# Kernel optimization log

Hardware: AMD Instinct MI355X
Metric: run time of the kernel (lower is better)

## Reference

```python
import jax, jax.numpy as jnp
import numpy as np

NEG_SLOPE = 0.01
EPS = 1e-8


def _conv2d(x, w, b, pad):
    y = jax.lax.conv_general_dilated(
        x, w, window_strides=(1, 1), padding=[(pad, pad), (pad, pad)],
        dimension_numbers=("NCHW", "OIHW", "NCHW"))
    return y + b[None, :, None, None]


def _leaky(x):
    return jnp.where(x >= 0, x, NEG_SLOPE * x)


def _maxpool2(x):
    return jax.lax.reduce_window(x, -jnp.inf, jax.lax.max,
                                 (1, 1, 2, 2), (1, 1, 2, 2), "VALID")


def _upsample2(x):  # nearest, scale_factor=2 (matches F.interpolate default)
    return jnp.repeat(jnp.repeat(x, 2, axis=2), 2, axis=3)


def _forward(x1, x2, pts1, enc, dec):
    B, L = pts1.shape[:2]
    H, W = x1.shape[-2:]
    h1, h2 = x1, x2
    pts = pts1.astype(jnp.int32)
    attns, feats = [], []
    for (w, b) in enc:
        Hi, Wi = h1.shape[-2:]
        h1 = _leaky(_conv2d(h1, w, b, 2))
        h2 = _leaky(_conv2d(h2, w, b, 2))
        feats.append(h2)
        h1 = _maxpool2(h1)
        h2 = _maxpool2(h2)
        C_, Hi_, Wi_ = h1.shape[-3:]
        # pts[...,0] = pts[...,0]*Hi_//Hi ; same for W (integer floor)
        pts = jnp.stack([(pts[..., 0] * Hi_) // Hi, (pts[..., 1] * Wi_) // Wi], axis=-1)
        idx = pts[..., 0] * Wi_ + pts[..., 1]  # (B, L)
        h1f = h1.reshape(B, C_, Hi_ * Wi_)
        h2f = h2.reshape(B, C_, Hi_ * Wi_)
        query = jnp.take_along_axis(h1f, jnp.broadcast_to(idx[:, None, :], (B, C_, L)), axis=2)  # (B, C, L)
        # cosine similarity between every pixel of h2 and every query point
        dots = jnp.einsum("bcp,bcl->bpl", h2f, query)
        n2 = jnp.maximum(jnp.linalg.norm(h2f, axis=1), EPS)    # (B, P)
        nq = jnp.maximum(jnp.linalg.norm(query, axis=1), EPS)  # (B, L)
        attn = dots / (n2[:, :, None] * nq[:, None, :])        # (B, P, L)
        attn = attn.reshape(B, Hi_, Wi_, L).transpose(0, 3, 1, 2).reshape(B * L, 1, Hi_, Wi_)
        attns.append(attn)
    h2 = jnp.tile(h2, (L, 1, 1, 1))  # torch .repeat(L,1,1,1)
    n_dec = len(dec)
    for i, (w, b) in enumerate(dec):
        j = len(enc) - i - 1
        h2 = jnp.concatenate([h2, attns[j]], axis=1)
        h2 = _upsample2(h2)
        feat = jnp.tile(feats[j], (L, 1, 1, 1))
        h2 = jnp.concatenate([h2, feat], axis=1)
        h2 = _conv2d(h2, w, b, 1)
        if i < n_dec - 1:
            h2 = _leaky(h2)
    return h2.reshape(B, L, H, W)


def setup_inputs() -> dict:
    key = jax.random.key(0)
    ks = jax.random.split(key, 24)
    B, L, H, W = 2, 32, 256, 256
    inp = {
        "x1": jax.random.uniform(ks[0], (B, 3, H, W), dtype=jnp.float32),
        "x2": jax.random.uniform(ks[1], (B, 3, H, W), dtype=jnp.float32),
        "pts1": jax.random.randint(ks[2], (B, L, 2), 0, H, dtype=jnp.int32),
    }
    enc_shapes = [(4, 3), (8, 4), (16, 8), (16, 16)]
    dec_shapes = [(16, 33), (8, 33), (4, 17), (1, 9)]
    k = 3
    for i, (co, ci) in enumerate(enc_shapes):
        inp[f"enc_w{i}"] = jax.random.normal(ks[k], (co, ci, 5, 5), dtype=jnp.float32) * 0.05
        inp[f"enc_b{i}"] = jnp.zeros((co,), dtype=jnp.float32)
        k += 1
    for i, (co, ci) in enumerate(dec_shapes):
        inp[f"dec_w{i}"] = jax.random.normal(ks[k], (co, ci, 3, 3), dtype=jnp.float32) * 0.05
        inp[f"dec_b{i}"] = jnp.zeros((co,), dtype=jnp.float32)
        k += 1
    return inp


def reference(x1, x2, pts1,
              enc_w0, enc_b0, enc_w1, enc_b1, enc_w2, enc_b2, enc_w3, enc_b3,
              dec_w0, dec_b0, dec_w1, dec_b1, dec_w2, dec_b2, dec_w3, dec_b3):
    enc = [(enc_w0, enc_b0), (enc_w1, enc_b1), (enc_w2, enc_b2), (enc_w3, enc_b3)]
    dec = [(dec_w0, dec_b0), (dec_w1, dec_b1), (dec_w2, dec_b2), (dec_w3, dec_b3)]
    return _forward(x1, x2, pts1, enc, dec)
```

## Files before the change

### kernel.cpp

```cpp
#include <hip/hip_runtime.h>
#include <cstdint>

__device__ __forceinline__ float leaky(float v) { return v >= 0.f ? v : 0.01f * v; }

__global__ void __launch_bounds__(256) enc0_k(
    const float* __restrict__ x1, const float* __restrict__ x2,
    const float* __restrict__ w, const float* __restrict__ bias,
    float* __restrict__ c2, float* __restrict__ pout)
{
    constexpr int R = 256;
    __shared__ float ss[3 * 36 * 36];
    __shared__ float ws[4 * 3 * 25 + 4];
    int t = threadIdx.x;
    int n = blockIdx.y;
    int tileY = blockIdx.x >> 3, tileX = blockIdx.x & 7;
    int Y0 = 32 * tileY, X0 = 32 * tileX;
    const float* src = (n < 2) ? x1 + (size_t)n * 3 * R * R
                               : x2 + (size_t)(n - 2) * 3 * R * R;

    for (int i = t; i < 300; i += 256) ws[i] = w[i];
    if (t < 4) ws[300 + t] = bias[t];
    for (int ci = 0; ci < 3; ++ci) {
        const float* sp = src + (size_t)ci * R * R;
        for (int i = t; i < 1296; i += 256) {
            int r = i / 36, col = i - r * 36;
            int gy = Y0 - 2 + r, gx = X0 - 2 + col;
            float v = 0.f;
            if (gy >= 0 && gy < R && gx >= 0 && gx < R) v = sp[gy * R + gx];
            ss[ci * 1296 + i] = v;
        }
    }
    __syncthreads();

    int qx = t & 15, qy = t >> 4;
    float acc[4][2][2];
#pragma unroll
    for (int co = 0; co < 4; ++co) {
        float b0 = ws[300 + co];
        acc[co][0][0] = b0; acc[co][0][1] = b0; acc[co][1][0] = b0; acc[co][1][1] = b0;
    }
#pragma unroll
    for (int ci = 0; ci < 3; ++ci) {
        const float* sp = &ss[ci * 1296 + (2 * qy) * 36 + 2 * qx];
        float S[6][6];
#pragma unroll
        for (int i = 0; i < 6; ++i)
#pragma unroll
            for (int j = 0; j < 6; ++j) S[i][j] = sp[i * 36 + j];
#pragma unroll
        for (int co = 0; co < 4; ++co) {
#pragma unroll
            for (int dy = 0; dy < 5; ++dy) {
#pragma unroll
                for (int dx = 0; dx < 5; ++dx) {
                    float wv = ws[(co * 3 + ci) * 25 + dy * 5 + dx];
                    acc[co][0][0] = fmaf(wv, S[dy][dx],         acc[co][0][0]);
                    acc[co][0][1] = fmaf(wv, S[dy][dx + 1],     acc[co][0][1]);
                    acc[co][1][0] = fmaf(wv, S[dy + 1][dx],     acc[co][1][0]);
                    acc[co][1][1] = fmaf(wv, S[dy + 1][dx + 1], acc[co][1][1]);
                }
            }
        }
    }
#pragma unroll
    for (int co = 0; co < 4; ++co) {
        float v00 = leaky(acc[co][0][0]), v01 = leaky(acc[co][0][1]);
        float v10 = leaky(acc[co][1][0]), v11 = leaky(acc[co][1][1]);
        if (n >= 2) {
            float* op = c2 + ((size_t)((n - 2) * 4 + co)) * R * R + (Y0 + 2 * qy) * R + X0 + 2 * qx;
            float2 a; a.x = v00; a.y = v01; *(float2*)op = a;
            float2 b2; b2.x = v10; b2.y = v11; *(float2*)(op + R) = b2;
        }
        float pv = fmaxf(fmaxf(v00, v01), fmaxf(v10, v11));
        pout[((size_t)(n * 4 + co)) * 16384 + (16 * tileY + qy) * 128 + 16 * tileX + qx] = pv;
    }
}

template<int R, int CI, int CO, int COG>
__global__ void __launch_bounds__(256) enc_k(
    const float* __restrict__ src1, const float* __restrict__ src2,
    const float* __restrict__ w, const float* __restrict__ bias,
    float* __restrict__ c2, float* __restrict__ pout)
{
    constexpr int W = R, H = R, Wt = R / 2;
    constexpr int RPB = 256 / Wt;
    __shared__ float ws[COG * CI * 25];
    __shared__ float pl[(RPB / 2) * COG * Wt];

    int t = threadIdx.x;
    int gid = blockIdx.x * 256 + t;
    int col = gid % Wt;
    int y = (gid / Wt) % H;
    int n = (gid / (Wt * H)) & 3;
    int g = gid / (Wt * H * 4);

    for (int i = t; i < COG * CI * 25; i += 256) ws[i] = w[g * COG * CI * 25 + i];
    __syncthreads();

    const float* sp = (n < 2) ? (src1 + (size_t)n * CI * H * W)
                              : (src2 + (size_t)(n - 2) * CI * H * W);
    int x0 = col * 2;

    float acc[COG][2];
#pragma unroll
    for (int cg = 0; cg < COG; ++cg) { float b0 = bias[g * COG + cg]; acc[cg][0] = b0; acc[cg][1] = b0; }

    bool okr[5], okc[3];
#pragma unroll
    for (int i = 0; i < 5; ++i) { int yy = y + i - 2; okr[i] = (yy >= 0) && (yy < H); }
#pragma unroll
    for (int j = 0; j < 3; ++j) { int xx = x0 + 2 * j - 2; okc[j] = (xx >= 0) && (xx < W); }

#pragma unroll 4
    for (int ci = 0; ci < CI; ++ci) {
        const float* s = sp + ci * H * W + (y - 2) * W + (x0 - 2);
        float p[5][6];
#pragma unroll
        for (int i = 0; i < 5; ++i) {
#pragma unroll
            for (int j = 0; j < 3; ++j) {
                if (okr[i] & okc[j]) {
                    float2 v = *(const float2*)(s + i * W + 2 * j);
                    p[i][2 * j] = v.x; p[i][2 * j + 1] = v.y;
                } else { p[i][2 * j] = 0.f; p[i][2 * j + 1] = 0.f; }
            }
        }
#pragma unroll
        for (int cg = 0; cg < COG; ++cg) {
#pragma unroll
            for (int dy = 0; dy < 5; ++dy) {
#pragma unroll
                for (int dx = 0; dx < 5; ++dx) {
                    float wv = ws[(cg * CI + ci) * 25 + dy * 5 + dx];
                    acc[cg][0] = fmaf(wv, p[dy][dx],     acc[cg][0]);
                    acc[cg][1] = fmaf(wv, p[dy][dx + 1], acc[cg][1]);
                }
            }
        }
    }

    int r = t / Wt;
    float m[COG];
#pragma unroll
    for (int cg = 0; cg < COG; ++cg) {
        float v0 = leaky(acc[cg][0]), v1 = leaky(acc[cg][1]);
        m[cg] = fmaxf(v0, v1);
        if (n >= 2) {
            float2 stv; stv.x = v0; stv.y = v1;
            *(float2*)(c2 + ((size_t)((n - 2) * CO + g * COG + cg)) * H * W + y * W + x0) = stv;
        }
    }
    if (r & 1) {
#pragma unroll
        for (int cg = 0; cg < COG; ++cg)
            pl[((r >> 1) * COG + cg) * Wt + col] = m[cg];
    }
    __syncthreads();
    if (!(r & 1)) {
#pragma unroll
        for (int cg = 0; cg < COG; ++cg) {
            float pv = fmaxf(m[cg], pl[((r >> 1) * COG + cg) * Wt + col]);
            pout[((size_t)(n * CO + g * COG + cg)) * Wt * Wt + (y >> 1) * Wt + col] = pv;
        }
    }
}

template<int C, int RP, int SHIFT>
__device__ __forceinline__ void attn_body(
    const float* __restrict__ pool, const int* __restrict__ pts,
    float* __restrict__ out, int tile, int b)
{
    constexpr int P = RP * RP;
    __shared__ float qs[32 * C];
    int t = threadIdx.x;
    if (t < 32) {
        int l = t;
        int py = pts[(b * 32 + l) * 2 + 0] >> SHIFT;
        int px = pts[(b * 32 + l) * 2 + 1] >> SHIFT;
        const float* qp = pool + (size_t)(b * C) * P + py * RP + px;
        float v[C]; float s = 0.f;
#pragma unroll
        for (int c = 0; c < C; ++c) { v[c] = qp[c * P]; s += v[c] * v[c]; }
        float invn = 1.f / fmaxf(sqrtf(s), 1e-8f);
#pragma unroll
        for (int c = 0; c < C; ++c) qs[l * C + c] = v[c] * invn;
    }
    __syncthreads();
    int p = tile * 256 + t;
    const float* hp = pool + (size_t)((2 + b) * C) * P + p;
    float v[C]; float s = 0.f;
#pragma unroll
    for (int c = 0; c < C; ++c) { v[c] = hp[c * P]; s += v[c] * v[c]; }
    float invn2 = 1.f / fmaxf(sqrtf(s), 1e-8f);
#pragma unroll 4
    for (int l = 0; l < 32; ++l) {
        float d = 0.f;
#pragma unroll
        for (int c = 0; c < C; ++c) d = fmaf(v[c], qs[l * C + c], d);
        out[(size_t)(b * 32 + l) * P + p] = d * invn2;
    }
}

__global__ void __launch_bounds__(256) attn_all_k(
    const float* __restrict__ p0, const float* __restrict__ p1,
    const float* __restrict__ p2, const float* __restrict__ p3,
    const int* __restrict__ pts,
    float* __restrict__ at0, float* __restrict__ at1,
    float* __restrict__ at2, float* __restrict__ at3)
{
    int bx = blockIdx.x;
    if (bx < 128)      attn_body<4, 128, 1>(p0, pts, at0, bx >> 1, bx & 1);
    else if (bx < 160) { int r = bx - 128; attn_body<8, 64, 2>(p1, pts, at1, r >> 1, r & 1); }
    else if (bx < 168) { int r = bx - 160; attn_body<16, 32, 3>(p2, pts, at2, r >> 1, r & 1); }
    else               { int r = bx - 168; attn_body<16, 16, 4>(p3, pts, at3, r >> 1, r & 1); }
}

template<int R, int CI, int CINW, int CO, int COG>
__device__ __forceinline__ void fb_body(
    const float* __restrict__ in, const float* __restrict__ w,
    const float* __restrict__ bias, float* __restrict__ fb,
    int par, int tile, int cog)
{
    constexpr int QD = R / 2;
    __shared__ float ws[COG * CI * 9];
    int t = threadIdx.x;
    for (int i = t; i < COG * CI * 9; i += 256) {
        int co = i / (CI * 9), rem = i - co * (CI * 9);
        ws[i] = w[(cog * COG + co) * CINW * 9 + (CINW - CI) * 9 + rem];
    }
    __syncthreads();
    int q = tile * 256 + t;
    int qx = q % QD, qy = q / QD;
    const float* ip = in + (size_t)par * CI * R * R;
    float acc[COG][2][2];
#pragma unroll
    for (int co = 0; co < COG; ++co) {
        float b0 = bias[cog * COG + co];
        acc[co][0][0] = b0; acc[co][0][1] = b0; acc[co][1][0] = b0; acc[co][1][1] = b0;
    }
    bool fr[4], fc[4];
#pragma unroll
    for (int i = 0; i < 4; ++i) {
        int yy = 2 * qy - 1 + i; fr[i] = (yy >= 0) && (yy < R);
        int xx = 2 * qx - 1 + i; fc[i] = (xx >= 0) && (xx < R);
    }
#pragma unroll 4
    for (int ci = 0; ci < CI; ++ci) {
        const float* bp = ip + (size_t)ci * R * R + (2 * qy - 1) * R + (2 * qx - 1);
        float F[4][4];
#pragma unroll
        for (int i = 0; i < 4; ++i)
#pragma unroll
            for (int j = 0; j < 4; ++j)
                F[i][j] = (fr[i] & fc[j]) ? bp[i * R + j] : 0.f;
#pragma unroll
        for (int co = 0; co < COG; ++co) {
#pragma unroll
            for (int dy = 0; dy < 3; ++dy) {
#pragma unroll
                for (int dx = 0; dx < 3; ++dx) {
                    float wv = ws[(co * CI + ci) * 9 + dy * 3 + dx];
                    acc[co][0][0] = fmaf(wv, F[dy][dx],         acc[co][0][0]);
                    acc[co][0][1] = fmaf(wv, F[dy][dx + 1],     acc[co][0][1]);
                    acc[co][1][0] = fmaf(wv, F[dy + 1][dx],     acc[co][1][0]);
                    acc[co][1][1] = fmaf(wv, F[dy + 1][dx + 1], acc[co][1][1]);
                }
            }
        }
    }
#pragma unroll
    for (int co = 0; co < COG; ++co) {
        float* op = fb + ((size_t)(par * CO + cog * COG + co)) * R * R + (2 * qy) * R + 2 * qx;
        float2 a; a.x = acc[co][0][0]; a.y = acc[co][0][1]; *(float2*)op = a;
        float2 b2; b2.x = acc[co][1][0]; b2.y = acc[co][1][1]; *(float2*)(op + R) = b2;
    }
}

__device__ __forceinline__ void fb0_body(
    const float* __restrict__ p3, const float* __restrict__ c2_3,
    const float* __restrict__ w, const float* __restrict__ bias,
    float* __restrict__ fb0, int par, int tile, int cog)
{
    __shared__ float ws0[4 * 33 * 9];
    int t = threadIdx.x;
    for (int i = t; i < 4 * 33 * 9; i += 256) ws0[i] = w[cog * 4 * 33 * 9 + i];
    __syncthreads();
    int px = tile * 256 + t;
    int x = px & 31, y = px >> 5;
    const float* prevp = p3 + (size_t)(2 + par) * 16 * 256;
    const float* featp = c2_3 + (size_t)par * 16 * 1024;
    float acc[4];
#pragma unroll
    for (int co = 0; co < 4; ++co) acc[co] = bias[cog * 4 + co];

    bool oky[3], okx[3];
    int py[3], pxh[3];
#pragma unroll
    for (int i = 0; i < 3; ++i) {
        int iy = y - 1 + i; oky[i] = (iy >= 0) && (iy < 32); py[i] = (iy >= 0 ? iy : 0) >> 1;
        int ix = x - 1 + i; okx[i] = (ix >= 0) && (ix < 32); pxh[i] = (ix >= 0 ? ix : 0) >> 1;
    }
#pragma unroll 4
    for (int ci = 0; ci < 16; ++ci) {
        const float* pp = prevp + ci * 256;
        float V[3][3];
#pragma unroll
        for (int i = 0; i < 3; ++i)
#pragma unroll
            for (int j = 0; j < 3; ++j)
                V[i][j] = (oky[i] & okx[j]) ? pp[py[i] * 16 + pxh[j]] : 0.f;
#pragma unroll
        for (int co = 0; co < 4; ++co) {
#pragma unroll
            for (int tap = 0; tap < 9; ++tap)
                acc[co] = fmaf(ws0[(co * 33 + ci) * 9 + tap], V[tap / 3][tap % 3], acc[co]);
        }
    }
#pragma unroll 4
    for (int cf = 0; cf < 16; ++cf) {
        const float* fp = featp + cf * 1024;
        float F[3][3];
#pragma unroll
        for (int i = 0; i < 3; ++i)
#pragma unroll
            for (int j = 0; j < 3; ++j) {
                int iy = y - 1 + i, ix = x - 1 + j;
                F[i][j] = (oky[i] & okx[j]) ? fp[iy * 32 + ix] : 0.f;
            }
#pragma unroll
        for (int co = 0; co < 4; ++co) {
#pragma unroll
            for (int tap = 0; tap < 9; ++tap)
                acc[co] = fmaf(ws0[(co * 33 + 17 + cf) * 9 + tap], F[tap / 3][tap % 3], acc[co]);
        }
    }
#pragma unroll
    for (int co = 0; co < 4; ++co)
        fb0[((size_t)(par * 16 + cog * 4 + co)) * 1024 + y * 32 + x] = acc[co];
}

__global__ void __launch_bounds__(256) fb_all_k(
    const float* __restrict__ p3, const float* __restrict__ c2_3,
    const float* __restrict__ c2_2, const float* __restrict__ c2_1,
    const float* __restrict__ c2_0,
    const float* __restrict__ w0, const float* __restrict__ b0,
    const float* __restrict__ w1, const float* __restrict__ b1,
    const float* __restrict__ w2, const float* __restrict__ b2,
    const float* __restrict__ w3, const float* __restrict__ b3,
    float* __restrict__ fb0, float* __restrict__ fb1,
    float* __restrict__ fb2, float* __restrict__ fb3)
{
    int bx = blockIdx.x;
    if (bx < 128) {
        int sub = bx; int par = sub >> 6, tile = sub & 63;
        fb_body<256, 4, 9, 1, 1>(c2_0, w3, b3, fb3, par, tile, 0);
    } else if (bx < 160) {
        int sub = bx - 128; int par = sub >> 4, tile = sub & 15;
        fb_body<128, 8, 17, 4, 4>(c2_1, w2, b2, fb2, par, tile, 0);
    } else if (bx < 176) {
        int sub = bx - 160; int cog = sub & 1, tile = (sub >> 1) & 3, par = sub >> 3;
        fb_body<64, 16, 33, 8, 4>(c2_2, w1, b1, fb1, par, tile, cog);
    } else {
        int sub = bx - 176; int cog = sub & 3, tile = (sub >> 2) & 3, par = sub >> 4;
        fb0_body(p3, c2_3, w0, b0, fb0, par, tile, cog);
    }
}

__global__ void __launch_bounds__(256) dec0k_k(
    const float* __restrict__ at3, const float* __restrict__ fb0,
    const float* __restrict__ w, float* __restrict__ out)
{
    __shared__ float ws4[9 * 16];
    int t = threadIdx.x;
    if (t < 144) {
        int tap = t / 16, co = t - (t / 16) * 16;
        ws4[tap * 16 + co] = w[co * 33 * 9 + 16 * 9 + tap];
    }
    __syncthreads();
    int gid = blockIdx.x;
    int k = gid >> 2, tile = gid & 3;
    int px = tile * 256 + t;
    int x = px & 31, y = px >> 5;
    int par = k & 1;
    const float* ap = at3 + (size_t)k * 256;

    float A[3][3];
#pragma unroll
    for (int i = 0; i < 3; ++i) {
        int iy = y - 1 + i; bool oy = (iy >= 0) && (iy < 32); int py = (iy >= 0 ? iy : 0) >> 1;
#pragma unroll
        for (int j = 0; j < 3; ++j) {
            int ix = x - 1 + j; bool ox = (ix >= 0) && (ix < 32); int qx = (ix >= 0 ? ix : 0) >> 1;
            A[i][j] = (oy && ox) ? ap[py * 16 + qx] : 0.f;
        }
    }
    float acc[16];
#pragma unroll
    for (int co = 0; co < 16; ++co)
        acc[co] = fb0[((size_t)(par * 16 + co)) * 1024 + y * 32 + x];
#pragma unroll
    for (int tap = 0; tap < 9; ++tap) {
        float av = A[tap / 3][tap % 3];
#pragma unroll
        for (int c4 = 0; c4 < 4; ++c4) {
            float4 wv = *(const float4*)&ws4[tap * 16 + c4 * 4];
            acc[c4 * 4 + 0] = fmaf(wv.x, av, acc[c4 * 4 + 0]);
            acc[c4 * 4 + 1] = fmaf(wv.y, av, acc[c4 * 4 + 1]);
            acc[c4 * 4 + 2] = fmaf(wv.z, av, acc[c4 * 4 + 2]);
            acc[c4 * 4 + 3] = fmaf(wv.w, av, acc[c4 * 4 + 3]);
        }
    }
#pragma unroll
    for (int co = 0; co < 16; ++co)
        out[((size_t)(k * 16 + co)) * 1024 + y * 32 + x] = leaky(acc[co]);
}

__global__ void __launch_bounds__(256, 4) dec1k_k(
    const float* __restrict__ prev, const float* __restrict__ attn,
    const float* __restrict__ fb1, const float* __restrict__ w,
    float* __restrict__ out)
{
    constexpr int R = 64, CP = 16, CIN = 33, Rh = 32, CO = 8, COG = 4;
    __shared__ float ws[17 * 9 * COG];
    __shared__ float sh4[17 * 60 * 4];

    int t = threadIdx.x;
    int bz = blockIdx.y;
    int kg = bz >> 1, cog = bz & 1;
    int p = kg & 1;
    int kbase = (kg >> 1) * 8 + p;
    int tileY = blockIdx.x >> 2, tileX = blockIdx.x & 3;
    int Y0 = 8 * tileY, X0 = 16 * tileX;
    int hy0 = 4 * tileY - 1, hx0 = 8 * tileX - 1;

    for (int i = t; i < 17 * 9 * COG; i += 256) {
        int col = i & 3, idx = i >> 2;
        ws[idx * 4 + col] = w[(cog * COG + col) * CIN * 9 + idx];
    }
#pragma unroll 2
    for (int i = t; i < 17 * 60; i += 256) {
        int c = i / 60, rem = i - c * 60;
        int r = rem / 10, col = rem - r * 10;
        int gy = hy0 + r, gx = hx0 + col;
        bool ok = (gy >= 0) && (gy < Rh) && (gx >= 0) && (gx < Rh);
        int off = gy * Rh + gx;
        float4 v4; v4.x = 0.f; v4.y = 0.f; v4.z = 0.f; v4.w = 0.f;
        if (ok) {
            if (c < CP) {
                v4.x = prev[((size_t)((kbase + 0) * CP + c)) * Rh * Rh + off];
                v4.y = prev[((size_t)((kbase + 2) * CP + c)) * Rh * Rh + off];
                v4.z = prev[((size_t)((kbase + 4) * CP + c)) * Rh * Rh + off];
                v4.w = prev[((size_t)((kbase + 6) * CP + c)) * Rh * Rh + off];
            } else {
                v4.x = attn[(size_t)(kbase + 0) * Rh * Rh + off];
                v4.y = attn[(size_t)(kbase + 2) * Rh * Rh + off];
                v4.z = attn[(size_t)(kbase + 4) * Rh * Rh + off];
                v4.w = attn[(size_t)(kbase + 6) * Rh * Rh + off];
            }
        }
        *(float4*)&sh4[i * 4] = v4;
    }
    __syncthreads();

    int px = t & 127, copair = t >> 7;
    int qx = px & 15, qy = px >> 4;

    float acc[4][2];
#pragma unroll
    for (int c2 = 0; c2 < 2; ++c2) {
        float fv = fb1[((size_t)(p * CO + cog * COG + copair * 2 + c2)) * 4096 + (Y0 + qy) * R + X0 + qx];
#pragma unroll
        for (int j = 0; j < 4; ++j) acc[j][c2] = fv;
    }

    int rr[3] = {(qy + 1) >> 1, (qy + 2) >> 1, (qy + 3) >> 1};
    int cc[3] = {(qx + 1) >> 1, (qx + 2) >> 1, (qx + 3) >> 1};
    int pofs[3][3];
#pragma unroll
    for (int i = 0; i < 3; ++i)
#pragma unroll
        for (int j2 = 0; j2 < 3; ++j2)
            pofs[i][j2] = (rr[i] * 10 + cc[j2]) * 4;

#pragma unroll 4
    for (int ci = 0; ci < 17; ++ci) {
        const float* hp = &sh4[ci * 240];
        float4 P4[3][3];
#pragma unroll
        for (int i = 0; i < 3; ++i)
#pragma unroll
            for (int j2 = 0; j2 < 3; ++j2)
                P4[i][j2] = *(const float4*)&hp[pofs[i][j2]];
#pragma unroll
        for (int dy = 0; dy < 3; ++dy) {
#pragma unroll
            for (int dx = 0; dx < 3; ++dx) {
                float2 wv = *(const float2*)&ws[(ci * 9 + dy * 3 + dx) * 4 + copair * 2];
                acc[0][0] = fmaf(wv.x, P4[dy][dx].x, acc[0][0]);
                acc[1][0] = fmaf(wv.x, P4[dy][dx].y, acc[1][0]);
                acc[2][0] = fmaf(wv.x, P4[dy][dx].z, acc[2][0]);
                acc[3][0] = fmaf(wv.x, P4[dy][dx].w, acc[3][0]);
                acc[0][1] = fmaf(wv.y, P4[dy][dx].x, acc[0][1]);
                acc[1][1] = fmaf(wv.y, P4[dy][dx].y, acc[1][1]);
                acc[2][1] = fmaf(wv.y, P4[dy][dx].z, acc[2][1]);
                acc[3][1] = fmaf(wv.y, P4[dy][dx].w, acc[3][1]);
            }
        }
    }

#pragma unroll
    for (int j = 0; j < 4; ++j) {
        int k = kbase + 2 * j;
#pragma unroll
        for (int c2 = 0; c2 < 2; ++c2) {
            int co = cog * COG + copair * 2 + c2;
            out[((size_t)(k * CO + co)) * 4096 + (Y0 + qy) * R + X0 + qx] = leaky(acc[j][c2]);
        }
    }
}

template<int R, int CP, int CO, int CINW, int MINW, bool DOLEAKY>
__global__ void __launch_bounds__(256, MINW) dechalf_k(
    const float* __restrict__ prev, const float* __restrict__ attn,
    const float* __restrict__ fb, const float* __restrict__ w,
    float* __restrict__ out)
{
    constexpr int Rh = R / 2, TX = R / 16;
    constexpr bool PACKW = (CO == 4);
    __shared__ float sh[4][(CP + 1) * 100];
    __shared__ float ws4[PACKW ? (CP + 1) * 9 * 4 : 4];

    int t = threadIdx.x;
    int kg = blockIdx.y;
    int p = kg & 1;
    int kbase = (kg >> 1) * 8 + p;
    int tileY = blockIdx.x / TX, tileX = blockIdx.x % TX;
    int Y0 = 16 * tileY, X0 = 16 * tileX;
    int hy0 = 8 * tileY - 1, hx0 = 8 * tileX - 1;

    if (PACKW) {
        for (int i = t; i < (CP + 1) * 9 * 4; i += 256) {
            int co = i & 3, idx = i >> 2;
            ws4[i] = w[co * CINW * 9 + idx];
        }
    }
#pragma unroll 2
    for (int i = t; i < CP * 100; i += 256) {
        int c = i / 100, rem = i - c * 100;
        int r = rem / 10, col = rem - r * 10;
        int gy = hy0 + r, gx = hx0 + col;
        bool ok = (gy >= 0) && (gy < Rh) && (gx >= 0) && (gx < Rh);
        int off = gy * Rh + gx;
#pragma unroll
        for (int j = 0; j < 4; ++j) {
            float v = 0.f;
            if (ok) v = prev[((size_t)((kbase + 2 * j) * CP + c)) * Rh * Rh + off];
            sh[j][i] = v;
        }
    }
    if (t < 100) {
        int r = t / 10, col = t - r * 10;
        int gy = hy0 + r, gx = hx0 + col;
        bool ok = (gy >= 0) && (gy < Rh) && (gx >= 0) && (gx < Rh);
        int off = gy * Rh + gx;
#pragma unroll
        for (int j = 0; j < 4; ++j) {
            float v = 0.f;
            if (ok) v = attn[(size_t)(kbase + 2 * j) * Rh * Rh + off];
            sh[j][CP * 100 + t] = v;
        }
    }
    __syncthreads();

    int ksub = t >> 6, q = t & 63, qx = q & 7, qy = q >> 3;
    int k = kbase + 2 * ksub;

    float acc[CO][2][2];
#pragma unroll
    for (int co = 0; co < CO; ++co) {
        const float* fp = fb + ((size_t)(p * CO + co)) * R * R + (Y0 + 2 * qy) * R + X0 + 2 * qx;
        float2 r0 = *(const float2*)fp;
        float2 r1 = *(const float2*)(fp + R);
        acc[co][0][0] = r0.x; acc[co][0][1] = r0.y;
        acc[co][1][0] = r1.x; acc[co][1][1] = r1.y;
    }

#pragma unroll
    for (int ci = 0; ci < CP + 1; ++ci) {
        const float* hp = &sh[ksub][ci * 100 + qy * 10 + qx];
        float P[3][3];
#pragma unroll
        for (int i = 0; i < 3; ++i)
#pragma unroll
            for (int j = 0; j < 3; ++j) P[i][j] = hp[i * 10 + j];
#pragma unroll
        for (int dy = 0; dy < 3; ++dy) {
#pragma unroll
            for (int dx = 0; dx < 3; ++dx) {
                float p00 = P[(dy + 1) >> 1][(dx + 1) >> 1];
                float p01 = P[(dy + 1) >> 1][(dx + 2) >> 1];
                float p10 = P[(dy + 2) >> 1][(dx + 1) >> 1];
                float p11 = P[(dy + 2) >> 1][(dx + 2) >> 1];
                if (PACKW) {
                    float4 wv = *(const float4*)&ws4[(ci * 9 + dy * 3 + dx) * 4];
                    const float* wvp = (const float*)&wv;
#pragma unroll
                    for (int co = 0; co < CO; ++co) {
                        acc[co][0][0] = fmaf(wvp[co], p00, acc[co][0][0]);
                        acc[co][0][1] = fmaf(wvp[co], p01, acc[co][0][1]);
                        acc[co][1][0] = fmaf(wvp[co], p10, acc[co][1][0]);
                        acc[co][1][1] = fmaf(wvp[co], p11, acc[co][1][1]);
                    }
                } else {
                    float wv = w[ci * 9 + dy * 3 + dx];
                    acc[0][0][0] = fmaf(wv, p00, acc[0][0][0]);
                    acc[0][0][1] = fmaf(wv, p01, acc[0][0][1]);
                    acc[0][1][0] = fmaf(wv, p10, acc[0][1][0]);
                    acc[0][1][1] = fmaf(wv, p11, acc[0][1][1]);
                }
            }
        }
    }

#pragma unroll
    for (int co = 0; co < CO; ++co) {
        float v00 = acc[co][0][0], v01 = acc[co][0][1];
        float v10 = acc[co][1][0], v11 = acc[co][1][1];
        if (DOLEAKY) { v00 = leaky(v00); v01 = leaky(v01); v10 = leaky(v10); v11 = leaky(v11); }
        float* op = out + ((size_t)(k * CO + co)) * R * R + (Y0 + 2 * qy) * R + X0 + 2 * qx;
        float2 a; a.x = v00; a.y = v01; *(float2*)op = a;
        float2 b2; b2.x = v10; b2.y = v11; *(float2*)(op + R) = b2;
    }
}

extern "C" void kernel_launch(void* const* d_in, const int* in_sizes, int n_in,
                              void* d_out, int out_size, void* d_ws, size_t ws_size,
                              hipStream_t stream)
{
    (void)in_sizes; (void)n_in; (void)out_size; (void)ws_size;
    const float* x1 = (const float*)d_in[0];
    const float* x2 = (const float*)d_in[1];
    const int* pts = (const int*)d_in[2];
    const float* ew[4] = {(const float*)d_in[3], (const float*)d_in[5],
                          (const float*)d_in[7], (const float*)d_in[9]};
    const float* eb[4] = {(const float*)d_in[4], (const float*)d_in[6],
                          (const float*)d_in[8], (const float*)d_in[10]};
    const float* dw[4] = {(const float*)d_in[11], (const float*)d_in[13],
                          (const float*)d_in[15], (const float*)d_in[17]};
    const float* db[4] = {(const float*)d_in[12], (const float*)d_in[14],
                          (const float*)d_in[16], (const float*)d_in[18]};

    float* wsp = (float*)d_ws;
    size_t off = 0;
    auto A = [&](size_t n) { float* p = wsp + off; off += n; return p; };

    float* p0 = A((size_t)4 * 4 * 128 * 128);
    float* p1 = A((size_t)4 * 8 * 64 * 64);
    float* p2 = A((size_t)4 * 16 * 32 * 32);
    float* p3 = A((size_t)4 * 16 * 16 * 16);
    float* c2_0 = A((size_t)2 * 4 * 256 * 256);
    float* c2_1 = A((size_t)2 * 8 * 128 * 128);
    float* c2_2 = A((size_t)2 * 16 * 64 * 64);
    float* c2_3 = A((size_t)2 * 16 * 32 * 32);
    float* at0 = A((size_t)64 * 128 * 128);
    float* at1 = A((size_t)64 * 64 * 64);
    float* at2 = A((size_t)64 * 32 * 32);
    float* at3 = A((size_t)64 * 16 * 16);
    float* dec0 = A((size_t)64 * 16 * 32 * 32);
    float* dec1 = A((size_t)64 * 8 * 64 * 64);
    float* dec2 = A((size_t)64 * 4 * 128 * 128);
    float* fb0 = A((size_t)2 * 16 * 32 * 32);
    float* fb1 = A((size_t)2 * 8 * 64 * 64);
    float* fb2 = A((size_t)2 * 4 * 128 * 128);
    float* fb3 = A((size_t)2 * 256 * 256);
    float* outp = (float*)d_out;

    { dim3 g(64, 4); enc0_k<<<g, 256, 0, stream>>>(x1, x2, ew[0], eb[0], c2_0, p0); }
    enc_k<128, 4, 8, 2><<<512, 256, 0, stream>>>(p0, p0 + (size_t)2 * 4 * 128 * 128,
                                                 ew[1], eb[1], c2_1, p1);
    enc_k<64, 8, 16, 2><<<256, 256, 0, stream>>>(p1, p1 + (size_t)2 * 8 * 64 * 64,
                                                 ew[2], eb[2], c2_2, p2);
    enc_k<32, 16, 16, 1><<<128, 256, 0, stream>>>(p2, p2 + (size_t)2 * 16 * 32 * 32,
                                                  ew[3], eb[3], c2_3, p3);

    attn_all_k<<<170, 256, 0, stream>>>(p0, p1, p2, p3, pts, at0, at1, at2, at3);

    fb_all_k<<<208, 256, 0, stream>>>(p3, c2_3, c2_2, c2_1, c2_0,
                                      dw[0], db[0], dw[1], db[1],
                                      dw[2], db[2], dw[3], db[3],
                                      fb0, fb1, fb2, fb3);

    dec0k_k<<<256, 256, 0, stream>>>(at3, fb0, dw[0], dec0);
    { dim3 g(32, 32); dec1k_k<<<g, 256, 0, stream>>>(dec0, at2, fb1, dw[1], dec1); }
    { dim3 g(64, 16); dechalf_k<128, 8, 4, 17, 4, true><<<g, 256, 0, stream>>>(dec1, at1, fb2, dw[2], dec2); }
    { dim3 g(256, 16); dechalf_k<256, 4, 1, 9, 5, false><<<g, 256, 0, stream>>>(dec2, at0, fb3, dw[3], outp); }
}
```

Before: 134.5 us.

## Merge last encoder stage with attention and feedback prep into fewer launches

Folds the last encoder conv, the attention maps for levels 0-2 and the feedback convs for levels 1-3 into one large kernel. Only the work that depends on p3 (level-3 attention and fb0) goes into a small second kernel. This cuts the three launches to two, regroups independent work so the GPU is better occupied, and places the two channel-group weights side by side in shared memory so enc_k can read them with float2 loads. The cost is a heavier fused kernel whose shared memory and register use is set by its largest branch, which may lower occupancy.

New measurement: 130.9 us, median of 2. 1.03x faster.

```diff
diff --git a/kernel.cpp b/kernel.cpp
--- a/kernel.cpp
+++ b/kernel.cpp
@@ -77,10 +77,10 @@
 }
 
 template<int R, int CI, int CO, int COG>
-__global__ void __launch_bounds__(256) enc_k(
+__device__ __forceinline__ void enc_body(
     const float* __restrict__ src1, const float* __restrict__ src2,
     const float* __restrict__ w, const float* __restrict__ bias,
-    float* __restrict__ c2, float* __restrict__ pout)
+    float* __restrict__ c2, float* __restrict__ pout, int bx)
 {
     constexpr int W = R, H = R, Wt = R / 2;
     constexpr int RPB = 256 / Wt;
@@ -88,13 +88,20 @@
     __shared__ float pl[(RPB / 2) * COG * Wt];
 
     int t = threadIdx.x;
-    int gid = blockIdx.x * 256 + t;
+    int gid = bx * 256 + t;
     int col = gid % Wt;
     int y = (gid / Wt) % H;
     int n = (gid / (Wt * H)) & 3;
     int g = gid / (Wt * H * 4);
 
-    for (int i = t; i < COG * CI * 25; i += 256) ws[i] = w[g * COG * CI * 25 + i];
+    if (COG == 2) {
+        for (int i = t; i < COG * CI * 25; i += 256) {
+            int cg = i & 1, idx = i >> 1;
+            ws[idx * 2 + cg] = w[(g * COG + cg) * CI * 25 + idx];
+        }
+    } else {
+        for (int i = t; i < COG * CI * 25; i += 256) ws[i] = w[g * COG * CI * 25 + i];
+    }
     __syncthreads();
 
     const float* sp = (n < 2) ? (src1 + (size_t)n * CI * H * W)
@@ -125,15 +132,29 @@
                 } else { p[i][2 * j] = 0.f; p[i][2 * j + 1] = 0.f; }
             }
         }
-#pragma unroll
-        for (int cg = 0; cg < COG; ++cg) {
+        if (COG == 2) {
 #pragma unroll
             for (int dy = 0; dy < 5; ++dy) {
 #pragma unroll
                 for (int dx = 0; dx < 5; ++dx) {
-                    float wv = ws[(cg * CI + ci) * 25 + dy * 5 + dx];
-                    acc[cg][0] = fmaf(wv, p[dy][dx],     acc[cg][0]);
-                    acc[cg][1] = fmaf(wv, p[dy][dx + 1], acc[cg][1]);
+                    float2 wv = *(const float2*)&ws[(ci * 25 + dy * 5 + dx) * 2];
+                    acc[0][0] = fmaf(wv.x, p[dy][dx],     acc[0][0]);
+                    acc[0][1] = fmaf(wv.x, p[dy][dx + 1], acc[0][1]);
+                    acc[1][0] = fmaf(wv.y, p[dy][dx],     acc[1][0]);
+                    acc[1][1] = fmaf(wv.y, p[dy][dx + 1], acc[1][1]);
+                }
+            }
+        } else {
+#pragma unroll
+            for (int cg = 0; cg < COG; ++cg) {
+#pragma unroll
+                for (int dy = 0; dy < 5; ++dy) {
+#pragma unroll
+                    for (int dx = 0; dx < 5; ++dx) {
+                        float wv = ws[(cg * CI + ci) * 25 + dy * 5 + dx];
+                        acc[cg][0] = fmaf(wv, p[dy][dx],     acc[cg][0]);
+                        acc[cg][1] = fmaf(wv, p[dy][dx + 1], acc[cg][1]);
+                    }
                 }
             }
         }
@@ -163,6 +184,15 @@
             pout[((size_t)(n * CO + g * COG + cg)) * Wt * Wt + (y >> 1) * Wt + col] = pv;
         }
     }
+}
+
+template<int R, int CI, int CO, int COG>
+__global__ void __launch_bounds__(256) enc_k(
+    const float* __restrict__ src1, const float* __restrict__ src2,
+    const float* __restrict__ w, const float* __restrict__ bias,
+    float* __restrict__ c2, float* __restrict__ pout)
+{
+    enc_body<R, CI, CO, COG>(src1, src2, w, bias, c2, pout, blockIdx.x);
 }
 
 template<int C, int RP, int SHIFT>
@@ -201,20 +231,6 @@
     }
 }
 
-__global__ void __launch_bounds__(256) attn_all_k(
-    const float* __restrict__ p0, const float* __restrict__ p1,
-    const float* __restrict__ p2, const float* __restrict__ p3,
-    const int* __restrict__ pts,
-    float* __restrict__ at0, float* __restrict__ at1,
-    float* __restrict__ at2, float* __restrict__ at3)
-{
-    int bx = blockIdx.x;
-    if (bx < 128)      attn_body<4, 128, 1>(p0, pts, at0, bx >> 1, bx & 1);
-    else if (bx < 160) { int r = bx - 128; attn_body<8, 64, 2>(p1, pts, at1, r >> 1, r & 1); }
-    else if (bx < 168) { int r = bx - 160; attn_body<16, 32, 3>(p2, pts, at2, r >> 1, r & 1); }
-    else               { int r = bx - 168; attn_body<16, 16, 4>(p3, pts, at3, r >> 1, r & 1); }
-}
-
 template<int R, int CI, int CINW, int CO, int COG>
 __device__ __forceinline__ void fb_body(
     const float* __restrict__ in, const float* __restrict__ w,
@@ -339,30 +355,52 @@
         fb0[((size_t)(par * 16 + cog * 4 + co)) * 1024 + y * 32 + x] = acc[co];
 }
 
-__global__ void __launch_bounds__(256) fb_all_k(
-    const float* __restrict__ p3, const float* __restrict__ c2_3,
-    const float* __restrict__ c2_2, const float* __restrict__ c2_1,
-    const float* __restrict__ c2_0,
-    const float* __restrict__ w0, const float* __restrict__ b0,
-    const float* __restrict__ w1, const float* __restrict__ b1,
-    const float* __restrict__ w2, const float* __restrict__ b2,
-    const float* __restrict__ w3, const float* __restrict__ b3,
-    float* __restrict__ fb0, float* __restrict__ fb1,
-    float* __restrict__ fb2, float* __restrict__ fb3)
+__global__ void __launch_bounds__(256) bigprep_k(
+    const float* __restrict__ p0, const float* __restrict__ p1,
+    const float* __restrict__ p2, const int* __restrict__ pts,
+    const float* __restrict__ ew3, const float* __restrict__ eb3,
+    float* __restrict__ c2_3, float* __restrict__ p3,
+    const float* __restrict__ c2_0, const float* __restrict__ c2_1,
+    const float* __restrict__ c2_2,
+    const float* __restrict__ dw1, const float* __restrict__ db1,
+    const float* __restrict__ dw2, const float* __restrict__ db2,
+    const float* __restrict__ dw3, const float* __restrict__ db3,
+    float* __restrict__ at0, float* __restrict__ at1, float* __restrict__ at2,
+    float* __restrict__ fb1, float* __restrict__ fb2, float* __restrict__ fb3)
 {
     int bx = blockIdx.x;
     if (bx < 128) {
-        int sub = bx; int par = sub >> 6, tile = sub & 63;
-        fb_body<256, 4, 9, 1, 1>(c2_0, w3, b3, fb3, par, tile, 0);
-    } else if (bx < 160) {
-        int sub = bx - 128; int par = sub >> 4, tile = sub & 15;
-        fb_body<128, 8, 17, 4, 4>(c2_1, w2, b2, fb2, par, tile, 0);
-    } else if (bx < 176) {
-        int sub = bx - 160; int cog = sub & 1, tile = (sub >> 1) & 3, par = sub >> 3;
-        fb_body<64, 16, 33, 8, 4>(c2_2, w1, b1, fb1, par, tile, cog);
+        enc_body<32, 16, 16, 1>(p2, p2 + (size_t)2 * 16 * 32 * 32, ew3, eb3, c2_3, p3, bx);
+    } else if (bx < 256) {
+        int r = bx - 128; attn_body<4, 128, 1>(p0, pts, at0, r >> 1, r & 1);
+    } else if (bx < 288) {
+        int r = bx - 256; attn_body<8, 64, 2>(p1, pts, at1, r >> 1, r & 1);
+    } else if (bx < 296) {
+        int r = bx - 288; attn_body<16, 32, 3>(p2, pts, at2, r >> 1, r & 1);
+    } else if (bx < 424) {
+        int sub = bx - 296; int par = sub >> 6, tile = sub & 63;
+        fb_body<256, 4, 9, 1, 1>(c2_0, dw3, db3, fb3, par, tile, 0);
+    } else if (bx < 456) {
+        int sub = bx - 424; int par = sub >> 4, tile = sub & 15;
+        fb_body<128, 8, 17, 4, 4>(c2_1, dw2, db2, fb2, par, tile, 0);
     } else {
-        int sub = bx - 176; int cog = sub & 3, tile = (sub >> 2) & 3, par = sub >> 4;
-        fb0_body(p3, c2_3, w0, b0, fb0, par, tile, cog);
+        int sub = bx - 456; int cog = sub & 1, tile = (sub >> 1) & 3, par = sub >> 3;
+        fb_body<64, 16, 33, 8, 4>(c2_2, dw1, db1, fb1, par, tile, cog);
+    }
+}
+
+__global__ void __launch_bounds__(256) prep2_k(
+    const float* __restrict__ p3, const float* __restrict__ c2_3,
+    const int* __restrict__ pts,
+    const float* __restrict__ dw0, const float* __restrict__ db0,
+    float* __restrict__ at3, float* __restrict__ fb0)
+{
+    int bx = blockIdx.x;
+    if (bx < 2) {
+        attn_body<16, 16, 4>(p3, pts, at3, bx >> 1, bx & 1);
+    } else {
+        int sub = bx - 2; int cog = sub & 3, tile = (sub >> 2) & 3, par = sub >> 4;
+        fb0_body(p3, c2_3, dw0, db0, fb0, par, tile, cog);
     }
 }
 
@@ -680,15 +718,13 @@
                                                  ew[1], eb[1], c2_1, p1);
     enc_k<64, 8, 16, 2><<<256, 256, 0, stream>>>(p1, p1 + (size_t)2 * 8 * 64 * 64,
                                                  ew[2], eb[2], c2_2, p2);
-    enc_k<32, 16, 16, 1><<<128, 256, 0, stream>>>(p2, p2 + (size_t)2 * 16 * 32 * 32,
-                                                  ew[3], eb[3], c2_3, p3);
-
-    attn_all_k<<<170, 256, 0, stream>>>(p0, p1, p2, p3, pts, at0, at1, at2, at3);
-
-    fb_all_k<<<208, 256, 0, stream>>>(p3, c2_3, c2_2, c2_1, c2_0,
-                                      dw[0], db[0], dw[1], db[1],
-                                      dw[2], db[2], dw[3], db[3],
-                                      fb0, fb1, fb2, fb3);
+
+    bigprep_k<<<472, 256, 0, stream>>>(p0, p1, p2, pts, ew[3], eb[3], c2_3, p3,
+                                       c2_0, c2_1, c2_2,
+                                       dw[1], db[1], dw[2], db[2], dw[3], db[3],
+                                       at0, at1, at2, fb1, fb2, fb3);
+
+    prep2_k<<<34, 256, 0, stream>>>(p3, c2_3, pts, dw[0], db[0], at3, fb0);
 
     dec0k_k<<<256, 256, 0, stream>>>(at3, fb0, dw[0], dec0);
     { dim3 g(32, 32); dec1k_k<<<g, 256, 0, stream>>>(dec0, at2, fb1, dw[1], dec1); }
```
